# Performance work log

Measured on AMD Instinct MI355X. Metric: run time of the kernel, lower is better.

## Reference

```python
import jax, jax.numpy as jnp
import numpy as np

HIDDEN = 1024
N_HEADS = 16
HEAD_DIM = HIDDEN // N_HEADS


def _rope_tables(seq_len, dim, dtype):
    inv_freq = 1.0 / (10000.0 ** (jnp.arange(0, dim, 2, dtype=jnp.float32) / dim))
    t = jnp.arange(seq_len, dtype=jnp.float32)
    freqs = jnp.einsum('i,j->ij', t, inv_freq)          # [S, dim/2]
    emb = jnp.concatenate([freqs, freqs], axis=-1)       # [S, dim]
    cos = jnp.cos(emb)[None, :, None, :].astype(dtype)   # [1, S, 1, dim]
    sin = jnp.sin(emb)[None, :, None, :].astype(dtype)
    return cos, sin


def _rotate_half(x):
    x1, x2 = x[..., : x.shape[-1] // 2], x[..., x.shape[-1] // 2 :]
    return jnp.concatenate([-x2, x1], axis=-1)


def setup_inputs() -> dict:
    key = jax.random.key(0)
    ks = jax.random.split(key, 9)
    s = 1.0 / np.sqrt(HIDDEN)
    return {
        'x': jax.random.normal(ks[0], (2, 2048, HIDDEN), dtype=jnp.float32),
        'q_w': jax.random.uniform(ks[1], (HIDDEN, HIDDEN), jnp.float32, -s, s),
        'q_b': jax.random.uniform(ks[2], (HIDDEN,), jnp.float32, -s, s),
        'k_w': jax.random.uniform(ks[3], (HIDDEN, HIDDEN), jnp.float32, -s, s),
        'k_b': jax.random.uniform(ks[4], (HIDDEN,), jnp.float32, -s, s),
        'v_w': jax.random.uniform(ks[5], (HIDDEN, HIDDEN), jnp.float32, -s, s),
        'v_b': jax.random.uniform(ks[6], (HIDDEN,), jnp.float32, -s, s),
        'o_w': jax.random.uniform(ks[7], (HIDDEN, HIDDEN), jnp.float32, -s, s),
        'o_b': jax.random.uniform(ks[8], (HIDDEN,), jnp.float32, -s, s),
    }


def reference(x, q_w, q_b, k_w, k_b, v_w, v_b, o_w, o_b):
    B, S, _ = x.shape
    scale = HEAD_DIM ** -0.5
    # projections (torch Linear: x @ W.T + b)
    q = (x @ q_w.T + q_b).reshape(B, S, N_HEADS, HEAD_DIM)
    k = (x @ k_w.T + k_b).reshape(B, S, N_HEADS, HEAD_DIM)
    v = (x @ v_w.T + v_b).reshape(B, S, N_HEADS, HEAD_DIM)
    # RoPE
    cos, sin = _rope_tables(S, HEAD_DIM, x.dtype)
    q = q * cos + _rotate_half(q) * sin
    k = k * cos + _rotate_half(k) * sin
    # attention: [B, H, S, S]
    scores = jnp.einsum('bqhd,bkhd->bhqk', q, k) * scale
    attn = jax.nn.softmax(scores, axis=-1)
    out = jnp.einsum('bhqk,bkhd->bqhd', attn, v).reshape(B, S, HIDDEN)
    return out @ o_w.T + o_b
```

## Files before the change

### kernel.cpp

```cpp
#include <hip/hip_runtime.h>
#include <hip/hip_bf16.h>


#define SEQ    2048
#define BATCH  2
#define NHEADS 16
#define HDIM   64
#define HID    1024
#define NTOK   (BATCH*SEQ)

typedef __bf16 bf16x8 __attribute__((ext_vector_type(8)));
typedef float  f32x4  __attribute__((ext_vector_type(4)));
typedef float  f32x16 __attribute__((ext_vector_type(16)));
typedef unsigned short u16x8 __attribute__((ext_vector_type(8)));
typedef unsigned int   u32x4 __attribute__((ext_vector_type(4)));

__device__ __forceinline__ unsigned short bfc(float x) {
  return __builtin_bit_cast(unsigned short, (__bf16)x);
}
__device__ __forceinline__ unsigned int pk(float lo, float hi) {
  return (unsigned int)bfc(lo) | ((unsigned int)bfc(hi) << 16);
}
__device__ __forceinline__ void plswap(unsigned int& a, unsigned int& b) {
  asm volatile("v_permlane32_swap_b32 %0, %1" : "+v"(a), "+v"(b));
}
#define EXP2(x) __builtin_amdgcn_exp2f(x)
#define MFMA32(a, b, c) __builtin_amdgcn_mfma_f32_32x32x16_bf16(a, b, c, 0, 0, 0)

__device__ __forceinline__ void gload16(const void* gptr, void* ldsptr) {
  typedef __attribute__((address_space(3))) unsigned int as3_uint;
  typedef const __attribute__((address_space(1))) unsigned int as1_uint;
  __builtin_amdgcn_global_load_lds(
      (as1_uint*)(unsigned long long)gptr,
      (as3_uint*)(unsigned int)(unsigned long long)ldsptr,
      16, 0, 0);
}

__device__ __forceinline__ void cvt8(const float* __restrict__ s,
                                     unsigned short* __restrict__ d, int i) {
  float4 a = *reinterpret_cast<const float4*>(s + i);
  float4 b = *reinterpret_cast<const float4*>(s + i + 4);
  u16x8 o;
  o[0] = bfc(a.x); o[1] = bfc(a.y); o[2] = bfc(a.z); o[3] = bfc(a.w);
  o[4] = bfc(b.x); o[5] = bfc(b.y); o[6] = bfc(b.z); o[7] = bfc(b.w);
  *reinterpret_cast<u16x8*>(d + i) = o;
}

__global__ __launch_bounds__(256) void prep(
    const float* __restrict__ x,
    const float* __restrict__ qw, const float* __restrict__ kw,
    const float* __restrict__ vw, const float* __restrict__ ow,
    unsigned short* __restrict__ xb,
    unsigned short* __restrict__ wqb, unsigned short* __restrict__ wkb,
    unsigned short* __restrict__ wvb, unsigned short* __restrict__ wob,
    float* __restrict__ ct, float* __restrict__ st)
{
  const int XN = NTOK * HID / 8;
  const int WN = HID * HID / 8;
  int tid = blockIdx.x * 256 + threadIdx.x;
  if (tid < XN) {
    cvt8(x, xb, tid * 8);
  } else if (tid < XN + 4 * WN) {
    int r = tid - XN;
    int which = r >> 17;
    int i = (r & (WN - 1)) * 8;
    const float* s = (which == 0) ? qw : (which == 1) ? kw : (which == 2) ? vw : ow;
    unsigned short* d = (which == 0) ? wqb : (which == 1) ? wkb : (which == 2) ? wvb : wob;
    cvt8(s, d, i);
  } else {
    int idx = tid - (XN + 4 * WN);
    if (idx < SEQ * 32) {
      int p = idx >> 5, j = idx & 31;
      float inv = powf(10000.0f, -(float)(2 * j) * (1.0f / 64.0f));
      float a = (float)p * inv;
      ct[idx] = cosf(a);
      st[idx] = sinf(a);
    }
  }
}

__global__ __launch_bounds__(256) void gemm_qkv(
    const unsigned short* __restrict__ X,
    const unsigned short* __restrict__ Wq, const unsigned short* __restrict__ Wk,
    const unsigned short* __restrict__ Wv,
    const float* __restrict__ bq, const float* __restrict__ bk, const float* __restrict__ bv,
    const float* __restrict__ ct, const float* __restrict__ st,
    unsigned short* __restrict__ Qo, unsigned short* __restrict__ Ko,
    unsigned short* __restrict__ VTo)
{
  __shared__ unsigned short LSH[24576];
  const int lin = blockIdx.x;
  const int swzb = (lin & 7) * 96 + (lin >> 3);
  const int z = swzb >> 8;
  const int tm = (swzb & 255) >> 3;
  const int tn = swzb & 7;
  const unsigned short* W = (z == 0) ? Wq : (z == 1) ? Wk : Wv;
  const float* bias = (z == 0) ? bq : (z == 1) ? bk : bv;
  const int t = threadIdx.x, w = t >> 6, l = t & 63;
  const int wm = w >> 1, wn = w & 1, g = l >> 4;

  f32x4 acc[4][4] = {};

  const int arow0 = tm * 128, brow0 = tn * 128;
  const int s0 = w * 2, s1 = w * 2 + 1;
  const int r0 = s0 * 16 + (l >> 2), r1 = s1 * 16 + (l >> 2);
  const int kc = (l & 3) * 8;

#define GSTAGE(buf, k0)                                                               \
  {                                                                                   \
    gload16(X + (long)(arow0 + r0) * HID + (k0) + kc, LSH + (buf) * 4096 + s0 * 512); \
    gload16(X + (long)(arow0 + r1) * HID + (k0) + kc, LSH + (buf) * 4096 + s1 * 512); \
    gload16(W + (long)(brow0 + r0) * HID + (k0) + kc, LSH + 12288 + (buf) * 4096 + s0 * 512); \
    gload16(W + (long)(brow0 + r1) * HID + (k0) + kc, LSH + 12288 + (buf) * 4096 + s1 * 512); \
  }

  GSTAGE(0, 0)
  GSTAGE(1, 32)
  asm volatile("s_waitcnt vmcnt(4)" ::: "memory");
  __builtin_amdgcn_s_barrier();
  int cur = 0, stg = 2;
  for (int k0 = 0; k0 < HID; k0 += 32) {
    if (k0 + 64 < HID) GSTAGE(stg, k0 + 64)
    bf16x8 af[4], bfr[4];
#pragma unroll
    for (int fm = 0; fm < 4; ++fm)
      af[fm] = *reinterpret_cast<const bf16x8*>(
          LSH + cur * 4096 + (wm * 64 + fm * 16 + (l & 15)) * 32 + g * 8);
#pragma unroll
    for (int fn = 0; fn < 4; ++fn)
      bfr[fn] = *reinterpret_cast<const bf16x8*>(
          LSH + 12288 + cur * 4096 + (wn * 64 + fn * 16 + (l & 15)) * 32 + g * 8);
    __builtin_amdgcn_s_setprio(1);
#pragma unroll
    for (int fm = 0; fm < 4; ++fm)
#pragma unroll
      for (int fn = 0; fn < 4; ++fn)
        acc[fm][fn] = __builtin_amdgcn_mfma_f32_16x16x32_bf16(af[fm], bfr[fn], acc[fm][fn], 0, 0, 0);
    __builtin_amdgcn_s_setprio(0);
    if (k0 + 64 < HID) {
      asm volatile("s_waitcnt vmcnt(4)" ::: "memory");
    } else {
      asm volatile("s_waitcnt vmcnt(0)" ::: "memory");
    }
    __builtin_amdgcn_s_barrier();
    cur = (cur == 2) ? 0 : cur + 1;
    stg = (stg == 2) ? 0 : stg + 1;
  }
#undef GSTAGE

  const int colb = brow0 + wn * 64;
  float bsv[4];
#pragma unroll
  for (int fn = 0; fn < 4; ++fn) bsv[fn] = bias[colb + fn * 16 + (l & 15)];

  if (z == 2) {
#pragma unroll
    for (int fm = 0; fm < 4; ++fm) {
      int tok = wm * 64 + fm * 16 + g * 4;
#pragma unroll
      for (int fn = 0; fn < 4; ++fn) {
        int col = wn * 64 + fn * 16 + (l & 15);
        unsigned int u0 = (unsigned int)bfc(acc[fm][fn][0] + bsv[fn]) |
                          ((unsigned int)bfc(acc[fm][fn][1] + bsv[fn]) << 16);
        unsigned int u1 = (unsigned int)bfc(acc[fm][fn][2] + bsv[fn]) |
                          ((unsigned int)bfc(acc[fm][fn][3] + bsv[fn]) << 16);
        uint2 uv; uv.x = u0; uv.y = u1;
        *reinterpret_cast<uint2*>(&LSH[col * 128 + (tok ^ ((col & 7) << 3))]) = uv;
      }
    }
    __syncthreads();
    const int bb = arow0 >> 11, stok = arow0 & (SEQ - 1);
#pragma unroll
    for (int p8 = 0; p8 < 8; ++p8) {
      int col = p8 * 16 + (t >> 4);
      int soff = (t & 15) * 8;
      uint4 v = *reinterpret_cast<const uint4*>(&LSH[col * 128 + (soff ^ ((col & 7) << 3))]);
      int hh = (brow0 + col) >> 6;
      int dd = col & 63;
      unsigned short* dst = VTo + ((long)(bb * NHEADS + hh) * HDIM + dd) * SEQ + stok + soff;
      *reinterpret_cast<uint4*>(dst) = v;
    }
    return;
  }

  unsigned short* Out = (z == 0) ? Qo : Ko;
  const int h = colb >> 6;
#pragma unroll
  for (int fm = 0; fm < 4; ++fm) {
#pragma unroll
    for (int r = 0; r < 4; ++r) {
      int grow = arow0 + wm * 64 + fm * 16 + g * 4 + r;
      int b = grow >> 11, sidx = grow & (SEQ - 1);
      unsigned short* ob = Out + ((long)(b * NHEADS + h) * SEQ + sidx) * HDIM;
#pragma unroll
      for (int fn2 = 0; fn2 < 2; ++fn2) {
        int d1 = fn2 * 16 + (l & 15);
        float v1 = acc[fm][fn2][r] + bsv[fn2];
        float v2 = acc[fm][fn2 + 2][r] + bsv[fn2 + 2];
        float c = ct[sidx * 32 + d1], sn = st[sidx * 32 + d1];
        float o1 = v1 * c - v2 * sn;
        float o2 = v2 * c + v1 * sn;
        if (z == 0) { o1 *= 0.18033688f; o2 *= 0.18033688f; }
        ob[d1] = bfc(o1);
        ob[d1 + 32] = bfc(o2);
      }
    }
  }
}

__global__ __launch_bounds__(256, 2) void attn(
    const unsigned short* __restrict__ Qb,
    const unsigned short* __restrict__ Kb,
    const unsigned short* __restrict__ VTb,
    unsigned short* __restrict__ Ob)
{
  __shared__ unsigned short Kl[2][128 * 64];
  __shared__ unsigned short Vl[3][8192];
  const int bh = blockIdx.x, qt = blockIdx.y;
  const int b = bh >> 4, h = bh & 15;
  const int t = threadIdx.x, w = t >> 6, l = t & 63;
  const long hb = (long)bh * SEQ * HDIM;
  const int hh = l >> 5;
  const int swz = (l & 7) << 4;

  const int q0 = qt * 128 + w * 32;
  bf16x8 qf[4];
#pragma unroll
  for (int dc = 0; dc < 4; ++dc)
    qf[dc] = *reinterpret_cast<const bf16x8*>(
        Qb + hb + (long)(q0 + (l & 31)) * HDIM + dc * 16 + hh * 8);

  f32x16 oacc[2] = {};
  f32x16 oaccE = {};
  const f32x16 FZ16 = {};

  u32x4 ou; ou[0] = 0x3F803F80u; ou[1] = 0x3F803F80u; ou[2] = 0x3F803F80u; ou[3] = 0x3F803F80u;
  const bf16x8 ones8 = __builtin_bit_cast(bf16x8, ou);

  const int srow = l >> 3;
  const int scol = (((l & 7) * 16) ^ ((l >> 3) << 4)) >> 1;
  const unsigned short* kp0 = Kb + hb + (long)(w * 32 + srow) * HDIM + scol;
  const unsigned short* kp1 = kp0 + 8 * HDIM;
  const unsigned short* kp2 = kp0 + 16 * HDIM;
  const unsigned short* kp3 = kp0 + 24 * HDIM;
  const unsigned short* vp0 = VTb + hb + (long)(w * 16 + srow) * SEQ + scol;
  const unsigned short* vp1 = vp0 + 8 * SEQ;
  const unsigned short* vp2 = vp0 + 64;
  const unsigned short* vp3 = vp1 + 64;

#define STAGE(kbuf, vbuf)                                                   \
  {                                                                         \
    gload16(kp0, (char*)Kl + (kbuf) * 16384 + w * 4096);                    \
    gload16(kp1, (char*)Kl + (kbuf) * 16384 + w * 4096 + 1024);             \
    gload16(kp2, (char*)Kl + (kbuf) * 16384 + w * 4096 + 2048);             \
    gload16(kp3, (char*)Kl + (kbuf) * 16384 + w * 4096 + 3072);             \
    gload16(vp0, (char*)Vl + (vbuf) * 16384 + w * 2048);                    \
    gload16(vp1, (char*)Vl + (vbuf) * 16384 + w * 2048 + 1024);             \
    gload16(vp2, (char*)Vl + (vbuf) * 16384 + 8192 + w * 2048);             \
    gload16(vp3, (char*)Vl + (vbuf) * 16384 + 8192 + w * 2048 + 1024);      \
    kp0 += 128 * HDIM; kp1 += 128 * HDIM; kp2 += 128 * HDIM; kp3 += 128 * HDIM; \
    vp0 += 128; vp1 += 128; vp2 += 128; vp3 += 128;                         \
  }

#define QK(kbuf)                                                                  \
  _Pragma("unroll")                                                               \
  for (int blk = 0; blk < 4; ++blk) {                                             \
    const char* kb_ = (char*)Kl + (kbuf) * 16384 + (32 * blk + (l & 31)) * 128;   \
    bf16x8 kf0 = *reinterpret_cast<const bf16x8*>(kb_ + ((0 * 32 + hh * 16) ^ swz)); \
    sa[blk] = MFMA32(kf0, qf[0], FZ16);                                           \
    bf16x8 kf1 = *reinterpret_cast<const bf16x8*>(kb_ + ((1 * 32 + hh * 16) ^ swz)); \
    sa[blk] = MFMA32(kf1, qf[1], sa[blk]);                                        \
    bf16x8 kf2 = *reinterpret_cast<const bf16x8*>(kb_ + ((2 * 32 + hh * 16) ^ swz)); \
    sa[blk] = MFMA32(kf2, qf[2], sa[blk]);                                        \
    bf16x8 kf3 = *reinterpret_cast<const bf16x8*>(kb_ + ((3 * 32 + hh * 16) ^ swz)); \
    sa[blk] = MFMA32(kf3, qf[3], sa[blk]);                                        \
  }

#define SOFTEXP                                                                   \
  _Pragma("unroll")                                                               \
  for (int blk = 0; blk < 4; ++blk)                                               \
    _Pragma("unroll")                                                             \
    for (int r = 0; r < 16; ++r) sa[blk][r] = EXP2(sa[blk][r]);

#define PBUILD                                                                    \
  _Pragma("unroll")                                                               \
  for (int blk = 0; blk < 4; ++blk) {                                             \
    unsigned int w0a = pk(sa[blk][0], sa[blk][1]);                                \
    unsigned int w1a = pk(sa[blk][2], sa[blk][3]);                                \
    unsigned int w0b = pk(sa[blk][4], sa[blk][5]);                                \
    unsigned int w1b = pk(sa[blk][6], sa[blk][7]);                                \
    unsigned int w0c = pk(sa[blk][8], sa[blk][9]);                                \
    unsigned int w1c = pk(sa[blk][10], sa[blk][11]);                              \
    unsigned int w0d = pk(sa[blk][12], sa[blk][13]);                              \
    unsigned int w1d = pk(sa[blk][14], sa[blk][15]);                              \
    plswap(w0a, w0b); plswap(w1a, w1b);                                           \
    plswap(w0c, w0d); plswap(w1c, w1d);                                           \
    u32x4 f0; f0[0] = w0a; f0[1] = w1a; f0[2] = w0b; f0[3] = w1b;                 \
    u32x4 f1; f1[0] = w0c; f1[1] = w1c; f1[2] = w0d; f1[3] = w1d;                 \
    pB[2 * blk + 0] = __builtin_bit_cast(bf16x8, f0);                             \
    pB[2 * blk + 1] = __builtin_bit_cast(bf16x8, f1);                             \
  }

#define PVSTEP(vbuf)                                                              \
  _Pragma("unroll")                                                               \
  for (int db = 0; db < 2; ++db) {                                                \
    _Pragma("unroll")                                                             \
    for (int kc = 0; kc < 8; ++kc) {                                              \
      const char* vb_ = (char*)Vl + (vbuf) * 16384 + (kc >> 2) * 8192 +           \
                        (32 * db + (l & 31)) * 128 + (((kc & 3) * 32 + hh * 16) ^ swz); \
      bf16x8 vf = *reinterpret_cast<const bf16x8*>(vb_);                          \
      oacc[db] = MFMA32(vf, pB[kc], oacc[db]);                                    \
    }                                                                             \
  }                                                                               \
  _Pragma("unroll")                                                               \
  for (int kc = 0; kc < 8; ++kc) oaccE = MFMA32(ones8, pB[kc], oaccE);

#define ITER(KB, VR, VW)                                   \
  {                                                        \
    STAGE(KB ^ 1, VW)                                      \
    __builtin_amdgcn_s_setprio(1);                         \
    QK(KB)                                                 \
    PVSTEP(VR)                                             \
    __builtin_amdgcn_s_setprio(0);                         \
    SOFTEXP                                                \
    PBUILD                                                 \
    asm volatile("s_waitcnt vmcnt(0)" ::: "memory");       \
    __builtin_amdgcn_s_barrier();                          \
  }
#define ITER_NOSTAGE(KB, VR)                               \
  {                                                        \
    __builtin_amdgcn_s_setprio(1);                         \
    QK(KB)                                                 \
    PVSTEP(VR)                                             \
    __builtin_amdgcn_s_setprio(0);                         \
    SOFTEXP                                                \
    PBUILD                                                 \
    asm volatile("s_waitcnt vmcnt(0)" ::: "memory");       \
    __builtin_amdgcn_s_barrier();                          \
  }

  f32x16 sa[4];
  bf16x8 pB[8];

  STAGE(0, 0)
  asm volatile("s_waitcnt vmcnt(0)" ::: "memory");
  __builtin_amdgcn_s_barrier();

  STAGE(1, 1)
  __builtin_amdgcn_s_setprio(1);
  QK(0)
  __builtin_amdgcn_s_setprio(0);
  SOFTEXP
  PBUILD
  asm volatile("s_waitcnt vmcnt(0)" ::: "memory");
  __builtin_amdgcn_s_barrier();

  for (int m = 0; m < 2; ++m) {
    ITER(1, 0, 2)
    ITER(0, 1, 0)
    ITER(1, 2, 1)
    ITER(0, 0, 2)
    ITER(1, 1, 0)
    ITER(0, 2, 1)
  }
  ITER(1, 0, 2)
  ITER(0, 1, 0)
  ITER_NOSTAGE(1, 2)

  __builtin_amdgcn_s_setprio(1);
  PVSTEP(0)
  __builtin_amdgcn_s_setprio(0);

#undef STAGE
#undef QK
#undef SOFTEXP
#undef PBUILD
#undef PVSTEP
#undef ITER
#undef ITER_NOSTAGE

  {
    float inv = 1.0f / oaccE[0];
    int q = q0 + (l & 31);
    unsigned short* op = Ob + (long)(b * SEQ + q) * HID + h * HDIM;
#pragma unroll
    for (int db = 0; db < 2; ++db)
#pragma unroll
      for (int a = 0; a < 4; ++a) {
        int d = 8 * a + 4 * hh + 32 * db;
        unsigned int lo = pk(oacc[db][4 * a + 0] * inv, oacc[db][4 * a + 1] * inv);
        unsigned int hi2 = pk(oacc[db][4 * a + 2] * inv, oacc[db][4 * a + 3] * inv);
        uint2 uv; uv.x = lo; uv.y = hi2;
        *reinterpret_cast<uint2*>(op + d) = uv;
      }
  }
}

__global__ __launch_bounds__(256) void gemm_o(
    const unsigned short* __restrict__ A,
    const unsigned short* __restrict__ W,
    const float* __restrict__ bias,
    float* __restrict__ Out)
{
  __shared__ unsigned short Al[3][128 * 32];
  __shared__ unsigned short Bl[3][64 * 32];
  const int lin = blockIdx.x;
  const int swzb = (lin & 7) * 64 + (lin >> 3);
  const int tm = swzb >> 4, tn = swzb & 15;
  const int t = threadIdx.x, w = t >> 6, l = t & 63;
  const int wm = w >> 1, wn = w & 1;

  f32x4 acc[4][2] = {};
  const int arow0 = tm * 128, brow0 = tn * 64;
  const int s0 = w * 2, s1 = w * 2 + 1;
  const int r0 = s0 * 16 + (l >> 2), r1 = s1 * 16 + (l >> 2);
  const int rb = w * 16 + (l >> 2);
  const int kc = (l & 3) * 8;

#define GSTAGE(buf, k0)                                                       \
  {                                                                           \
    gload16(A + (long)(arow0 + r0) * HID + (k0) + kc, Al[buf] + s0 * 512);    \
    gload16(A + (long)(arow0 + r1) * HID + (k0) + kc, Al[buf] + s1 * 512);    \
    gload16(W + (long)(brow0 + rb) * HID + (k0) + kc, Bl[buf] + w * 512);     \
  }

  GSTAGE(0, 0)
  GSTAGE(1, 32)
  asm volatile("s_waitcnt vmcnt(3)" ::: "memory");
  __builtin_amdgcn_s_barrier();
  int cur = 0, stg = 2;
  for (int k0 = 0; k0 < HID; k0 += 32) {
    if (k0 + 64 < HID) GSTAGE(stg, k0 + 64)
    bf16x8 af[4], bfr[2];
#pragma unroll
    for (int fm = 0; fm < 4; ++fm)
      af[fm] = *reinterpret_cast<const bf16x8*>(Al[cur] + (wm * 64 + fm * 16 + (l & 15)) * 32 + (l >> 4) * 8);
#pragma unroll
    for (int fn = 0; fn < 2; ++fn)
      bfr[fn] = *reinterpret_cast<const bf16x8*>(Bl[cur] + (wn * 32 + fn * 16 + (l & 15)) * 32 + (l >> 4) * 8);
    __builtin_amdgcn_s_setprio(1);
#pragma unroll
    for (int fm = 0; fm < 4; ++fm)
#pragma unroll
      for (int fn = 0; fn < 2; ++fn)
        acc[fm][fn] = __builtin_amdgcn_mfma_f32_16x16x32_bf16(af[fm], bfr[fn], acc[fm][fn], 0, 0, 0);
    __builtin_amdgcn_s_setprio(0);
    if (k0 + 64 < HID) {
      asm volatile("s_waitcnt vmcnt(3)" ::: "memory");
    } else {
      asm volatile("s_waitcnt vmcnt(0)" ::: "memory");
    }
    __builtin_amdgcn_s_barrier();
    cur = (cur == 2) ? 0 : cur + 1;
    stg = (stg == 2) ? 0 : stg + 1;
  }
#undef GSTAGE

  const int colb = brow0 + wn * 32;
  float bsv[2];
#pragma unroll
  for (int fn = 0; fn < 2; ++fn) bsv[fn] = bias[colb + fn * 16 + (l & 15)];
#pragma unroll
  for (int fm = 0; fm < 4; ++fm)
#pragma unroll
    for (int r = 0; r < 4; ++r) {
      int grow = arow0 + wm * 64 + fm * 16 + (l >> 4) * 4 + r;
#pragma unroll
      for (int fn = 0; fn < 2; ++fn)
        Out[(long)grow * HID + colb + fn * 16 + (l & 15)] = acc[fm][fn][r] + bsv[fn];
    }
}

extern "C" void kernel_launch(void* const* d_in, const int* in_sizes, int n_in,
                              void* d_out, int out_size, void* d_ws, size_t ws_size,
                              hipStream_t stream) {
  const float* x  = (const float*)d_in[0];
  const float* qw = (const float*)d_in[1];
  const float* qb = (const float*)d_in[2];
  const float* kw = (const float*)d_in[3];
  const float* kb = (const float*)d_in[4];
  const float* vw = (const float*)d_in[5];
  const float* vb = (const float*)d_in[6];
  const float* ow = (const float*)d_in[7];
  const float* ob = (const float*)d_in[8];
  float* out = (float*)d_out;

  char* p = (char*)d_ws;
  unsigned short* xb  = (unsigned short*)p; p += (size_t)NTOK * HID * 2;
  unsigned short* wqb = (unsigned short*)p; p += (size_t)HID * HID * 2;
  unsigned short* wkb = (unsigned short*)p; p += (size_t)HID * HID * 2;
  unsigned short* wvb = (unsigned short*)p; p += (size_t)HID * HID * 2;
  unsigned short* wob = (unsigned short*)p; p += (size_t)HID * HID * 2;
  unsigned short* Qb  = (unsigned short*)p; p += (size_t)NTOK * HID * 2;
  unsigned short* Kb  = (unsigned short*)p; p += (size_t)NTOK * HID * 2;
  unsigned short* VTb = (unsigned short*)p; p += (size_t)NTOK * HID * 2;
  float* ct = (float*)p; p += (size_t)SEQ * 32 * 4;
  float* st = (float*)p; p += (size_t)SEQ * 32 * 4;
  unsigned short* Ab  = xb;

  const int XN = NTOK * HID / 8, WN = HID * HID / 8;
  const int prep_threads = XN + 4 * WN + SEQ * 32;
  prep<<<dim3((prep_threads + 255) / 256), 256, 0, stream>>>(
      x, qw, kw, vw, ow, xb, wqb, wkb, wvb, wob, ct, st);

  gemm_qkv<<<dim3(768), 256, 0, stream>>>(
      xb, wqb, wkb, wvb, qb, kb, vb, ct, st, Qb, Kb, VTb);

  attn<<<dim3(BATCH * NHEADS, SEQ / 128), 256, 0, stream>>>(Qb, Kb, VTb, Ab);

  gemm_o<<<dim3(512), 256, 0, stream>>>(Ab, wob, ob, out);
}
```

Before: 113.9 us.

## Rework QKV and output GEMMs to BK=64 double-buffered XOR-swizzled LDS tiles

Both projection GEMMs move from a triple-buffered BK=32 pipeline to a double-buffered BK=64 pipeline with an XOR-swizzled LDS layout meant to avoid bank conflicts on the fragment reads. This halves the number of barriers per K sweep. The block-index swizzle for L2 locality is replaced by a plain 2D/3D grid, and launch bounds gain a minimum-blocks hint. In exchange, each iteration now waits for vmcnt(0), which exposes more load latency, and the plain grid may lose cache reuse.

Result: faster. 104.4 us (-8.4%).

```diff
diff --git a/kernel.cpp b/kernel.cpp
--- a/kernel.cpp
+++ b/kernel.cpp
@@ -79,7 +79,7 @@
   }
 }
 
-__global__ __launch_bounds__(256) void gemm_qkv(
+__global__ __launch_bounds__(256, 2) void gemm_qkv(
     const unsigned short* __restrict__ X,
     const unsigned short* __restrict__ Wq, const unsigned short* __restrict__ Wk,
     const unsigned short* __restrict__ Wv,
@@ -88,63 +88,65 @@
     unsigned short* __restrict__ Qo, unsigned short* __restrict__ Ko,
     unsigned short* __restrict__ VTo)
 {
-  __shared__ unsigned short LSH[24576];
-  const int lin = blockIdx.x;
-  const int swzb = (lin & 7) * 96 + (lin >> 3);
-  const int z = swzb >> 8;
-  const int tm = (swzb & 255) >> 3;
-  const int tn = swzb & 7;
+  __shared__ unsigned short LSH[32768];
+  const int z = blockIdx.z;
   const unsigned short* W = (z == 0) ? Wq : (z == 1) ? Wk : Wv;
   const float* bias = (z == 0) ? bq : (z == 1) ? bk : bv;
+  const int tm = blockIdx.x, tn = blockIdx.y;
   const int t = threadIdx.x, w = t >> 6, l = t & 63;
   const int wm = w >> 1, wn = w & 1, g = l >> 4;
+  const int swz = (l & 7) << 4;
 
   f32x4 acc[4][4] = {};
 
   const int arow0 = tm * 128, brow0 = tn * 128;
-  const int s0 = w * 2, s1 = w * 2 + 1;
-  const int r0 = s0 * 16 + (l >> 2), r1 = s1 * 16 + (l >> 2);
-  const int kc = (l & 3) * 8;
-
-#define GSTAGE(buf, k0)                                                               \
-  {                                                                                   \
-    gload16(X + (long)(arow0 + r0) * HID + (k0) + kc, LSH + (buf) * 4096 + s0 * 512); \
-    gload16(X + (long)(arow0 + r1) * HID + (k0) + kc, LSH + (buf) * 4096 + s1 * 512); \
-    gload16(W + (long)(brow0 + r0) * HID + (k0) + kc, LSH + 12288 + (buf) * 4096 + s0 * 512); \
-    gload16(W + (long)(brow0 + r1) * HID + (k0) + kc, LSH + 12288 + (buf) * 4096 + s1 * 512); \
+  const int srow = l >> 3;
+  const int scol = (((l & 7) * 16) ^ ((l >> 3) << 4)) >> 1;
+
+#define GSTAGE(buf, k0)                                                             \
+  {                                                                                 \
+    _Pragma("unroll")                                                               \
+    for (int c = 0; c < 4; ++c)                                                     \
+      gload16(X + (long)(arow0 + w * 32 + c * 8 + srow) * HID + (k0) + scol,        \
+              (char*)LSH + (buf) * 16384 + w * 4096 + c * 1024);                    \
+    _Pragma("unroll")                                                               \
+    for (int c = 0; c < 4; ++c)                                                     \
+      gload16(W + (long)(brow0 + w * 32 + c * 8 + srow) * HID + (k0) + scol,        \
+              (char*)LSH + 32768 + (buf) * 16384 + w * 4096 + c * 1024);            \
   }
 
   GSTAGE(0, 0)
-  GSTAGE(1, 32)
-  asm volatile("s_waitcnt vmcnt(4)" ::: "memory");
+  asm volatile("s_waitcnt vmcnt(0)" ::: "memory");
   __builtin_amdgcn_s_barrier();
-  int cur = 0, stg = 2;
-  for (int k0 = 0; k0 < HID; k0 += 32) {
-    if (k0 + 64 < HID) GSTAGE(stg, k0 + 64)
-    bf16x8 af[4], bfr[4];
-#pragma unroll
-    for (int fm = 0; fm < 4; ++fm)
-      af[fm] = *reinterpret_cast<const bf16x8*>(
-          LSH + cur * 4096 + (wm * 64 + fm * 16 + (l & 15)) * 32 + g * 8);
-#pragma unroll
-    for (int fn = 0; fn < 4; ++fn)
-      bfr[fn] = *reinterpret_cast<const bf16x8*>(
-          LSH + 12288 + cur * 4096 + (wn * 64 + fn * 16 + (l & 15)) * 32 + g * 8);
-    __builtin_amdgcn_s_setprio(1);
-#pragma unroll
-    for (int fm = 0; fm < 4; ++fm)
-#pragma unroll
-      for (int fn = 0; fn < 4; ++fn)
-        acc[fm][fn] = __builtin_amdgcn_mfma_f32_16x16x32_bf16(af[fm], bfr[fn], acc[fm][fn], 0, 0, 0);
-    __builtin_amdgcn_s_setprio(0);
-    if (k0 + 64 < HID) {
-      asm volatile("s_waitcnt vmcnt(4)" ::: "memory");
-    } else {
-      asm volatile("s_waitcnt vmcnt(0)" ::: "memory");
-    }
+  int cur = 0;
+  for (int k0 = 0; k0 < HID; k0 += 64) {
+    if (k0 + 64 < HID) GSTAGE(cur ^ 1, k0 + 64)
+#pragma unroll
+    for (int kk = 0; kk < 2; ++kk) {
+      bf16x8 af[4], bfr[4];
+#pragma unroll
+      for (int fm = 0; fm < 4; ++fm) {
+        int row = wm * 64 + fm * 16 + (l & 15);
+        af[fm] = *reinterpret_cast<const bf16x8*>(
+            (char*)LSH + cur * 16384 + row * 128 + ((kk * 64 + g * 16) ^ swz));
+      }
+#pragma unroll
+      for (int fn = 0; fn < 4; ++fn) {
+        int row = wn * 64 + fn * 16 + (l & 15);
+        bfr[fn] = *reinterpret_cast<const bf16x8*>(
+            (char*)LSH + 32768 + cur * 16384 + row * 128 + ((kk * 64 + g * 16) ^ swz));
+      }
+      __builtin_amdgcn_s_setprio(1);
+#pragma unroll
+      for (int fm = 0; fm < 4; ++fm)
+#pragma unroll
+        for (int fn = 0; fn < 4; ++fn)
+          acc[fm][fn] = __builtin_amdgcn_mfma_f32_16x16x32_bf16(af[fm], bfr[fn], acc[fm][fn], 0, 0, 0);
+      __builtin_amdgcn_s_setprio(0);
+    }
+    asm volatile("s_waitcnt vmcnt(0)" ::: "memory");
     __builtin_amdgcn_s_barrier();
-    cur = (cur == 2) ? 0 : cur + 1;
-    stg = (stg == 2) ? 0 : stg + 1;
+    cur ^= 1;
   }
 #undef GSTAGE
 
@@ -396,63 +398,68 @@
   }
 }
 
-__global__ __launch_bounds__(256) void gemm_o(
+__global__ __launch_bounds__(256, 3) void gemm_o(
     const unsigned short* __restrict__ A,
     const unsigned short* __restrict__ W,
     const float* __restrict__ bias,
     float* __restrict__ Out)
 {
-  __shared__ unsigned short Al[3][128 * 32];
-  __shared__ unsigned short Bl[3][64 * 32];
-  const int lin = blockIdx.x;
-  const int swzb = (lin & 7) * 64 + (lin >> 3);
-  const int tm = swzb >> 4, tn = swzb & 15;
+  __shared__ unsigned short Al[2][128 * 64];
+  __shared__ unsigned short Bl[2][64 * 64];
+  const int tm = blockIdx.x, tn = blockIdx.y;
   const int t = threadIdx.x, w = t >> 6, l = t & 63;
-  const int wm = w >> 1, wn = w & 1;
+  const int wm = w >> 1, wn = w & 1, g = l >> 4;
+  const int swz = (l & 7) << 4;
 
   f32x4 acc[4][2] = {};
   const int arow0 = tm * 128, brow0 = tn * 64;
-  const int s0 = w * 2, s1 = w * 2 + 1;
-  const int r0 = s0 * 16 + (l >> 2), r1 = s1 * 16 + (l >> 2);
-  const int rb = w * 16 + (l >> 2);
-  const int kc = (l & 3) * 8;
-
-#define GSTAGE(buf, k0)                                                       \
-  {                                                                           \
-    gload16(A + (long)(arow0 + r0) * HID + (k0) + kc, Al[buf] + s0 * 512);    \
-    gload16(A + (long)(arow0 + r1) * HID + (k0) + kc, Al[buf] + s1 * 512);    \
-    gload16(W + (long)(brow0 + rb) * HID + (k0) + kc, Bl[buf] + w * 512);     \
+  const int srow = l >> 3;
+  const int scol = (((l & 7) * 16) ^ ((l >> 3) << 4)) >> 1;
+
+#define GSTAGE(buf, k0)                                                             \
+  {                                                                                 \
+    _Pragma("unroll")                                                               \
+    for (int c = 0; c < 4; ++c)                                                     \
+      gload16(A + (long)(arow0 + w * 32 + c * 8 + srow) * HID + (k0) + scol,        \
+              (char*)Al + (buf) * 16384 + w * 4096 + c * 1024);                     \
+    _Pragma("unroll")                                                               \
+    for (int c = 0; c < 2; ++c)                                                     \
+      gload16(W + (long)(brow0 + w * 16 + c * 8 + srow) * HID + (k0) + scol,        \
+              (char*)Bl + (buf) * 8192 + w * 2048 + c * 1024);                      \
   }
 
   GSTAGE(0, 0)
-  GSTAGE(1, 32)
-  asm volatile("s_waitcnt vmcnt(3)" ::: "memory");
+  asm volatile("s_waitcnt vmcnt(0)" ::: "memory");
   __builtin_amdgcn_s_barrier();
-  int cur = 0, stg = 2;
-  for (int k0 = 0; k0 < HID; k0 += 32) {
-    if (k0 + 64 < HID) GSTAGE(stg, k0 + 64)
-    bf16x8 af[4], bfr[2];
-#pragma unroll
-    for (int fm = 0; fm < 4; ++fm)
-      af[fm] = *reinterpret_cast<const bf16x8*>(Al[cur] + (wm * 64 + fm * 16 + (l & 15)) * 32 + (l >> 4) * 8);
-#pragma unroll
-    for (int fn = 0; fn < 2; ++fn)
-      bfr[fn] = *reinterpret_cast<const bf16x8*>(Bl[cur] + (wn * 32 + fn * 16 + (l & 15)) * 32 + (l >> 4) * 8);
-    __builtin_amdgcn_s_setprio(1);
-#pragma unroll
-    for (int fm = 0; fm < 4; ++fm)
-#pragma unroll
-      for (int fn = 0; fn < 2; ++fn)
-        acc[fm][fn] = __builtin_amdgcn_mfma_f32_16x16x32_bf16(af[fm], bfr[fn], acc[fm][fn], 0, 0, 0);
-    __builtin_amdgcn_s_setprio(0);
-    if (k0 + 64 < HID) {
-      asm volatile("s_waitcnt vmcnt(3)" ::: "memory");
-    } else {
-      asm volatile("s_waitcnt vmcnt(0)" ::: "memory");
-    }
+  int cur = 0;
+  for (int k0 = 0; k0 < HID; k0 += 64) {
+    if (k0 + 64 < HID) GSTAGE(cur ^ 1, k0 + 64)
+#pragma unroll
+    for (int kk = 0; kk < 2; ++kk) {
+      bf16x8 af[4], bfr[2];
+#pragma unroll
+      for (int fm = 0; fm < 4; ++fm) {
+        int row = wm * 64 + fm * 16 + (l & 15);
+        af[fm] = *reinterpret_cast<const bf16x8*>(
+            (char*)Al + cur * 16384 + row * 128 + ((kk * 64 + g * 16) ^ swz));
+      }
+#pragma unroll
+      for (int fn = 0; fn < 2; ++fn) {
+        int row = wn * 32 + fn * 16 + (l & 15);
+        bfr[fn] = *reinterpret_cast<const bf16x8*>(
+            (char*)Bl + cur * 8192 + row * 128 + ((kk * 64 + g * 16) ^ swz));
+      }
+      __builtin_amdgcn_s_setprio(1);
+#pragma unroll
+      for (int fm = 0; fm < 4; ++fm)
+#pragma unroll
+        for (int fn = 0; fn < 2; ++fn)
+          acc[fm][fn] = __builtin_amdgcn_mfma_f32_16x16x32_bf16(af[fm], bfr[fn], acc[fm][fn], 0, 0, 0);
+      __builtin_amdgcn_s_setprio(0);
+    }
+    asm volatile("s_waitcnt vmcnt(0)" ::: "memory");
     __builtin_amdgcn_s_barrier();
-    cur = (cur == 2) ? 0 : cur + 1;
-    stg = (stg == 2) ? 0 : stg + 1;
+    cur ^= 1;
   }
 #undef GSTAGE
 
@@ -503,10 +510,10 @@
   prep<<<dim3((prep_threads + 255) / 256), 256, 0, stream>>>(
       x, qw, kw, vw, ow, xb, wqb, wkb, wvb, wob, ct, st);
 
-  gemm_qkv<<<dim3(768), 256, 0, stream>>>(
+  gemm_qkv<<<dim3(NTOK / 128, HID / 128, 3), 256, 0, stream>>>(
       xb, wqb, wkb, wvb, qb, kb, vb, ct, st, Qb, Kb, VTb);
 
   attn<<<dim3(BATCH * NHEADS, SEQ / 128), 256, 0, stream>>>(Qb, Kb, VTb, Ab);
 
-  gemm_o<<<dim3(512), 256, 0, stream>>>(Ab, wob, ob, out);
-}
+  gemm_o<<<dim3(NTOK / 128, HID / 64), 256, 0, stream>>>(Ab, wob, ob, out);
+}
```
